# Optimization experiments

Hardware: AMD Instinct MI355X
Metric: run time of the kernel (lower is better)

## Reference

```python
import jax, jax.numpy as jnp
import numpy as np

WIDTH = 384
STEP_SIZE = 0.1  # hard-coded in EnergyBlock.__init__
EPS = 1e-5


def conv1d(x, w):
    # x: [B, Cin, L], w: [Cout, Cin, K], stride 1, SAME padding (padding=1 for k=3)
    return jax.lax.conv_general_dilated(
        x, w, window_strides=(1,), padding='SAME',
        dimension_numbers=('NCH', 'OIH', 'NCH'))


def layer_norm_cl(x):
    # torch layer_norm over shape[1:] == normalize jointly over (C, L) per batch elem,
    # no affine params, biased variance.
    mu = jnp.mean(x, axis=(1, 2), keepdims=True)
    var = jnp.mean(jnp.square(x - mu), axis=(1, 2), keepdims=True)
    return (x - mu) * jax.lax.rsqrt(var + EPS)


def energy_block(cat, op_w):
    # cat: [B, width+1, L] = concat(interim_thought, x)
    xl = layer_norm_cl(cat[:, :WIDTH])          # post-LN x (the grad variable)
    c = conv1d(cat, op_w)                        # operator(inputs): no path through xl
    # Ex = sum(c * xl) + sum(where(xl>=0, xl^2, 0))
    # dEx/dxl = c + 2*relu(xl)  (analytic; matches torch.autograd.grad)
    grads = c + 2.0 * jnp.maximum(xl, 0.0)
    return xl - STEP_SIZE * grads


def _init_conv(key, cout, cin, k=3):
    scale = (1.0 / (cin * k)) ** 0.5
    return jax.random.uniform(key, (cout, cin, k), jnp.float32, -scale, scale)


def setup_inputs() -> dict:
    key = jax.random.key(0)
    ks = jax.random.split(key, 6)
    B, L = 32, 512
    return {
        'x': jax.random.normal(ks[0], (B, 1, L), jnp.float32),
        'iters_to_do': 16,
        'proj_w': _init_conv(ks[1], WIDTH, 1),
        'op_w': _init_conv(ks[2], WIDTH, WIDTH + 1),
        'h1_w': _init_conv(ks[3], WIDTH, WIDTH),
        'h2_w': _init_conv(ks[4], WIDTH // 2, WIDTH),
        'h3_w': _init_conv(ks[5], 2, WIDTH // 2),
    }


def reference(x, iters_to_do, proj_w, op_w, h1_w, h2_w, h3_w):
    relu = jax.nn.relu
    interim = relu(conv1d(x, proj_w))  # initial_thought [B, width, L]

    def step(it, _):
        cat = jnp.concatenate([it, x], axis=1)       # recall=True
        new_it = energy_block(cat, op_w)
        out = conv1d(relu(conv1d(relu(conv1d(new_it, h1_w)), h2_w)), h3_w)  # [B,2,L]
        return new_it, out

    _, outs = jax.lax.scan(step, interim, None, length=iters_to_do)
    # eval mode: return all_outputs [B, iters, 2, L]
    return jnp.transpose(outs, (1, 0, 2, 3))
```

## Files before the change

### kernel.cpp

```cpp
#include <hip/hip_runtime.h>
#include <hip/hip_bf16.h>

#define BB 32
#define WW 384
#define LL 512
#define ITERS 16
#define NPB (WW * LL)
#define LROWS 514
#define RP (LROWS * 8)

typedef __attribute__((ext_vector_type(8))) short bf16x8;
typedef __attribute__((ext_vector_type(4))) float f32x4;

__device__ __forceinline__ float b2f(short s) {
    unsigned u = ((unsigned)(unsigned short)s) << 16;
    float f;
    __builtin_memcpy(&f, &u, 4);
    return f;
}
__device__ __forceinline__ short f2b(float v) {
    __hip_bfloat16 h = __float2bfloat16(v);
    return *(short*)&h;
}

__device__ __forceinline__ void gld16(const short* g, short* l) {
    __builtin_amdgcn_global_load_lds(
        (const __attribute__((address_space(1))) unsigned int*)g,
        (__attribute__((address_space(3))) unsigned int*)l, 16, 0, 0);
}

__global__ void wsplit_op(const float* __restrict__ w, short* __restrict__ wh) {
    int i = blockIdx.x * 256 + threadIdx.x;
    if (i >= 3 * 48 * 384 * 8) return;
    int e = i & 7, co = (i >> 3) % 384, oct = (i >> 3) / 384 % 48,
        tap = i / (8 * 384 * 48);
    int ci = oct * 8 + e;
    wh[i] = f2b(w[(co * 385 + ci) * 3 + tap]);
}

__global__ void wx_prep(const float* __restrict__ w, float* __restrict__ wx) {
    int i = blockIdx.x * 256 + threadIdx.x;
    if (i >= 3 * 384) return;
    int co = i % 384, tap = i / 384;
    wx[tap * 384 + co] = w[(co * 385 + 384) * 3 + tap];
}

__global__ void wsplit_h(const float* __restrict__ w, short* __restrict__ wh,
                         int COD, int CO_real) {
    int i = blockIdx.x * 256 + threadIdx.x;
    if (i >= 3 * 48 * COD * 8) return;
    int e = i & 7, co = (i >> 3) % COD, oct = (i >> 3) / COD % 48,
        tap = i / (8 * COD * 48);
    int ci = oct * 8 + e;
    float v = (co < CO_real) ? w[(co * 384 + ci) * 3 + tap] : 0.f;
    wh[i] = f2b(v);
}

__global__ void init_rows(short* itAh, short* itAl, short* itBh, short* itBl,
                          short* a1A, short* a1B, short* a2A, short* a2B) {
    int row = (blockIdx.x & 1) ? (LROWS - 1) : 0;
    int b = blockIdx.x >> 1;
    int tid = threadIdx.x;
    for (int i = tid; i < 48 * 8; i += 64) {
        size_t o = (size_t)b * 48 * RP + (size_t)(i >> 3) * RP + row * 8 + (i & 7);
        itAh[o] = 0; itAl[o] = 0; itBh[o] = 0; itBl[o] = 0;
        a1A[o] = 0; a1B[o] = 0;
    }
    for (int i = tid; i < 24 * 8; i += 64) {
        size_t o = (size_t)b * 24 * RP + (size_t)(i >> 3) * RP + row * 8 + (i & 7);
        a2A[o] = 0; a2B[o] = 0;
    }
}

__global__ void zero_part(float* part, int n) {
    int i = blockIdx.x * 256 + threadIdx.x;
    if (i < n) part[i] = 0.f;
}

__global__ __launch_bounds__(256) void proj_relu(const float* __restrict__ x,
                                                 const float* __restrict__ wp,
                                                 short* __restrict__ oh,
                                                 short* __restrict__ ol,
                                                 float* __restrict__ part) {
    int b = blockIdx.x >> 3, sl = blockIdx.x & 7;
    int tid = threadIdx.x;
    __shared__ float ws[WW * 3];
    __shared__ float xs[66];
    for (int i = tid; i < WW * 3; i += 256) ws[i] = wp[i];
    int l0 = sl * 64;
    for (int i = tid; i < 66; i += 256) {
        int l = l0 + i - 1;
        xs[i] = (l >= 0 && l < LL) ? x[b * LL + l] : 0.f;
    }
    __syncthreads();
    size_t sb = (size_t)b * 48 * RP;
    float s = 0.f, sq = 0.f;
    for (int idx = tid; idx < 64 * WW; idx += 256) {
        int lo = idx / WW, co = idx % WW;
        float v = fmaxf(ws[co * 3] * xs[lo] + ws[co * 3 + 1] * xs[lo + 1] +
                            ws[co * 3 + 2] * xs[lo + 2], 0.f);
        size_t o = sb + (size_t)(co >> 3) * RP + (l0 + lo + 1) * 8 + (co & 7);
        __hip_bfloat16 h = __float2bfloat16(v);
        oh[o] = *(short*)&h;
        ol[o] = f2b(v - __bfloat162float(h));
        s += v; sq += v * v;
    }
    #pragma unroll
    for (int off = 32; off > 0; off >>= 1) {
        s += __shfl_down(s, off);
        sq += __shfl_down(sq, off);
    }
    __shared__ float sr[8];
    int w = tid >> 6;
    if ((tid & 63) == 0) { sr[w] = s; sr[4 + w] = sq; }
    __syncthreads();
    if (tid == 0) {
        atomicAdd(&part[b * 2], sr[0] + sr[1] + sr[2] + sr[3]);
        atomicAdd(&part[b * 2 + 1], sr[4] + sr[5] + sr[6] + sr[7]);
    }
}


#define MMAC(A, B, MT, NT)                                                 \
    acc[MT][NT] = __builtin_amdgcn_mfma_f32_16x16x32_bf16(A, B,            \
                                                          acc[MT][NT], 0, 0, 0);

#define STAGE(KC, TB)                                                      \
    do {                                                                   \
        short* sb_ = smem + (TB) * (ASZ + BSZ);                            \
        _Pragma("unroll")                                                  \
        for (int r_ = 0; r_ < (ANS + 3) / 4; r_++) {                       \
            int s_ = r_ * 4 + wn;                                          \
            if (s_ < ANS) {                                                \
                int u0_ = s_ * 64;                                         \
                if (u0_ > AU - 64) u0_ = AU - 64;                          \
                int u_ = u0_ + lane;                                       \
                int oc_ = u_ / TLROWS;                                     \
                int rw_ = u_ - oc_ * TLROWS;                               \
                gld16(inh + ibase + (size_t)((KC) * 4 + oc_) * RP +        \
                          (size_t)(l0 + rw_) * 8,                          \
                      sb_ + u0_ * 8);                                      \
            }                                                              \
        }                                                                  \
        _Pragma("unroll")                                                  \
        for (int r_ = 0; r_ < BNS / 4; r_++) {                            \
            int u0_ = (r_ * 4 + wn) * 64;                                  \
            int t_ = u0_ / (4 * TCO);                                      \
            int rq_ = (u0_ / TCO) & 3;                                     \
            int co_ = (u0_ & (TCO - 1)) + lane;                            \
            gld16(wh + ((((size_t)t_ * CHUNKS + (KC)) * 4 + rq_) * COD +   \
                        co0 + co_) * 8,                                    \
                  sb_ + ASZ + u0_ * 8);                                    \
        }                                                                  \
    } while (0)

#define COMP_TAP(SB, T)                                                    \
    do {                                                                   \
        const short* As_ = (SB);                                           \
        const short* Bs_ = (SB) + ASZ;                                     \
        int ar_ = q * TLROWS + wl + lane15 + (T);                          \
        bf16x8 fa0 = *(const bf16x8*)(As_ + ar_ * 8);                      \
        bf16x8 fa1 = *(const bf16x8*)(As_ + (ar_ + 16) * 8);               \
        bf16x8 fa2 = *(const bf16x8*)(As_ + (ar_ + 32) * 8);               \
        bf16x8 fa3 = *(const bf16x8*)(As_ + (ar_ + 48) * 8);               \
        int br_ = ((T) * 4 + q) * TCO + wco + lane15;                      \
        bf16x8 fb0 = *(const bf16x8*)(Bs_ + br_ * 8);                      \
        bf16x8 fb1 = *(const bf16x8*)(Bs_ + (br_ + 16) * 8);               \
        bf16x8 fb2 = *(const bf16x8*)(Bs_ + (br_ + 32) * 8);               \
        bf16x8 fb3 = *(const bf16x8*)(Bs_ + (br_ + 48) * 8);               \
        MMAC(fa0, fb0, 0, 0) MMAC(fa0, fb1, 0, 1)                          \
        MMAC(fa0, fb2, 0, 2) MMAC(fa0, fb3, 0, 3)                          \
        MMAC(fa1, fb0, 1, 0) MMAC(fa1, fb1, 1, 1)                          \
        MMAC(fa1, fb2, 1, 2) MMAC(fa1, fb3, 1, 3)                          \
        MMAC(fa2, fb0, 2, 0) MMAC(fa2, fb1, 2, 1)                          \
        MMAC(fa2, fb2, 2, 2) MMAC(fa2, fb3, 2, 3)                          \
        MMAC(fa3, fb0, 3, 0) MMAC(fa3, fb1, 3, 1)                          \
        MMAC(fa3, fb2, 3, 2) MMAC(fa3, fb3, 3, 3)                          \
    } while (0)

template <int CHUNKS, int IOCT, int OOCT, int COD, int MODE, int LSPLIT>
__device__ __forceinline__ void conv_body(
    int bid, short* smem,
    const short* __restrict__ inh, const short* __restrict__ inl,
    const short* __restrict__ wh, const float* __restrict__ xf,
    const float* __restrict__ wx, const float* __restrict__ part_in,
    float* __restrict__ part_out, short* __restrict__ outh,
    short* __restrict__ outl) {
    constexpr int TLROWS = LSPLIT ? 258 : 130;
    constexpr int TCO = LSPLIT ? 64 : 128;
    constexpr int ASZ = 4 * TLROWS * 8;
    constexpr int BSZ = 12 * TCO * 8;
    constexpr int AU = 4 * TLROWS;
    constexpr int ANS = (AU + 63) / 64;
    constexpr int BNS = (12 * TCO) / 64;

    int tid = threadIdx.x;
    int lane = tid & 63;
    int wn = __builtin_amdgcn_readfirstlane(tid >> 6);
    int lane15 = lane & 15, q = lane >> 4;
    int b, l0, co0, wl, wco;
    if (LSPLIT) {
        int ct = bid >> 6, g = bid & 63;
        b = g >> 1; l0 = (g & 1) * 256; co0 = ct * 64;
        wl = wn * 64; wco = 0;
    } else {
        int ct = bid >> 7, g = bid & 127;
        b = g >> 2; l0 = (g & 3) * 128; co0 = ct * 128;
        wl = (wn >> 1) * 64; wco = (wn & 1) * 64;
    }
    const size_t ibase = (size_t)b * IOCT * RP;

    f32x4 acc[4][4];
    #pragma unroll
    for (int i = 0; i < 4; i++)
        #pragma unroll
        for (int j = 0; j < 4; j++) acc[i][j] = (f32x4){0.f, 0.f, 0.f, 0.f};

    STAGE(0, 0);
    __syncthreads();
    #pragma unroll 2
    for (int kc = 0; kc < CHUNKS; kc++) {
        int cur = kc & 1;
        if (kc + 1 < CHUNKS) STAGE(kc + 1, cur ^ 1);
        short* sb = smem + cur * (ASZ + BSZ);
        COMP_TAP(sb, 0);
        COMP_TAP(sb, 1);
        COMP_TAP(sb, 2);
        __syncthreads();
    }

    int l0w = l0 + wl, co0w = co0 + wco;
    const size_t obase = (size_t)b * OOCT * RP;
    if constexpr (MODE == 1) {
        float s_in = part_in[b * 2], sq_in = part_in[b * 2 + 1];
        float mu = s_in / (float)NPB;
        float var = sq_in / (float)NPB - mu * mu;
        float rs = rsqrtf(var + 1e-5f);
        const float* xb = xf + b * LL;
        float s = 0.f, sq = 0.f;
        #pragma unroll
        for (int nt = 0; nt < 4; nt++) {
            int n = co0w + nt * 16 + lane15;
            float w0 = wx[n], w1 = wx[384 + n], w2 = wx[768 + n];
            #pragma unroll
            for (int mt = 0; mt < 4; mt++)
                #pragma unroll
                for (int r = 0; r < 4; r++) {
                    int m = mt * 16 + q * 4 + r;
                    int l = l0w + m;
                    size_t idx = ibase + (size_t)(n >> 3) * RP +
                                 (l + 1) * 8 + (n & 7);
                    float xm1 = (l > 0) ? xb[l - 1] : 0.f;
                    float xp1 = (l < LL - 1) ? xb[l + 1] : 0.f;
                    float c = acc[mt][nt][r] + w0 * xm1 + w1 * xb[l] + w2 * xp1;
                    float itv = b2f(inh[idx]) + b2f(inl[idx]);
                    float xl = (itv - mu) * rs;
                    float nv = xl - 0.1f * c - 0.2f * fmaxf(xl, 0.f);
                    s += nv;
                    sq += nv * nv;
                    __hip_bfloat16 h = __float2bfloat16(nv);
                    outh[idx] = *(short*)&h;
                    outl[idx] = f2b(nv - __bfloat162float(h));
                }
        }
        #pragma unroll
        for (int off = 32; off > 0; off >>= 1) {
            s += __shfl_down(s, off);
            sq += __shfl_down(sq, off);
        }
        __shared__ float sr[8];
        if (lane == 0) { sr[wn] = s; sr[4 + wn] = sq; }
        __syncthreads();
        if (tid == 0) {
            atomicAdd(&part_out[b * 2], sr[0] + sr[1] + sr[2] + sr[3]);
            atomicAdd(&part_out[b * 2 + 1], sr[4] + sr[5] + sr[6] + sr[7]);
        }
    } else {
        #pragma unroll
        for (int mt = 0; mt < 4; mt++)
            #pragma unroll
            for (int nt = 0; nt < 4; nt++)
                #pragma unroll
                for (int r = 0; r < 4; r++) {
                    int m = mt * 16 + q * 4 + r;
                    int n = co0w + nt * 16 + lane15;
                    size_t idx = obase + (size_t)(n >> 3) * RP +
                                 (l0w + m + 1) * 8 + (n & 7);
                    outh[idx] = f2b(fmaxf(acc[mt][nt][r], 0.f));
                }
    }
}

__global__ __launch_bounds__(128) void h3k(const short* __restrict__ a2,
                                           const float* __restrict__ w3,
                                           float* __restrict__ out, int t) {
    __shared__ float ws3[2 * 192 * 3];
    int tid = threadIdx.x;
    for (int i = tid; i < 2 * 192 * 3; i += 128) ws3[i] = w3[i];
    __syncthreads();
    int b = blockIdx.x >> 3, sl = blockIdx.x & 7;
    int l = sl * 64 + (tid >> 1);
    int ch = tid & 1;
    const short* ab = a2 + (size_t)b * 24 * RP;
    const float* wc = ws3 + ch * 576;
    float a = 0.f;
    #pragma unroll 4
    for (int oct = 0; oct < 24; oct++) {
        const short* p = ab + (size_t)oct * RP + l * 8;
        bf16x8 v0 = *(const bf16x8*)p;
        bf16x8 v1 = *(const bf16x8*)(p + 8);
        bf16x8 v2 = *(const bf16x8*)(p + 16);
        #pragma unroll
        for (int j = 0; j < 8; j++) {
            const float* wp = wc + (oct * 8 + j) * 3;
            a += wp[0] * b2f(v0[j]) + wp[1] * b2f(v1[j]) + wp[2] * b2f(v2[j]);
        }
    }
    out[(((size_t)b * ITERS + t) * 2 + ch) * LL + l] = a;
}

__global__ __launch_bounds__(256, 2) void fusedF(
    const short* __restrict__ ch, const short* __restrict__ cl,
    short* __restrict__ nh, short* __restrict__ nl,
    const short* __restrict__ wOph, const short* __restrict__ wH1,
    const short* __restrict__ wH2, const float* __restrict__ xf,
    const float* __restrict__ wx, const float* __restrict__ part_in,
    float* __restrict__ part_out, short* __restrict__ a1w,
    const short* __restrict__ a1r, short* __restrict__ a2w,
    int opB, int h1B) {
    __shared__ __align__(16) short smem[2 * (4 * 130 * 8 + 12 * 128 * 8)];
    int bid = blockIdx.x;
    if (bid < opB) {
        conv_body<12, 48, 48, 384, 1, 0>(bid, smem, ch, cl, wOph, xf, wx,
                                         part_in, part_out, nh, nl);
    } else if (bid < opB + h1B) {
        conv_body<12, 48, 48, 384, 0, 0>(bid - opB, smem, ch, nullptr, wH1,
                                         nullptr, nullptr, nullptr, nullptr,
                                         a1w, nullptr);
    } else {
        conv_body<12, 48, 24, 192, 0, 1>(bid - opB - h1B, smem, a1r, nullptr,
                                         wH2, nullptr, nullptr, nullptr,
                                         nullptr, a2w, nullptr);
    }
}

extern "C" void kernel_launch(void* const* d_in, const int* in_sizes, int n_in,
                              void* d_out, int out_size, void* d_ws, size_t ws_size,
                              hipStream_t stream) {
    const float* x = (const float*)d_in[0];
    const float* proj_w = (const float*)d_in[2];
    const float* op_w = (const float*)d_in[3];
    const float* h1_w = (const float*)d_in[4];
    const float* h2_w = (const float*)d_in[5];
    const float* h3_w = (const float*)d_in[6];
    float* out = (float*)d_out;

    char* base = (char*)d_ws;
    size_t off = 0;
    auto alloc = [&](size_t bytes) {
        char* p = base + off;
        off += (bytes + 255) & ~(size_t)255;
        return p;
    };
    const size_t ITB = (size_t)BB * 48 * RP * 2;
    short* itAh = (short*)alloc(ITB);
    short* itAl = (short*)alloc(ITB);
    short* itBh = (short*)alloc(ITB);
    short* itBl = (short*)alloc(ITB);
    short* a1A = (short*)alloc((size_t)BB * 48 * RP * 2);
    short* a1B = (short*)alloc((size_t)BB * 48 * RP * 2);
    short* a2A = (short*)alloc((size_t)BB * 24 * RP * 2);
    short* a2B = (short*)alloc((size_t)BB * 24 * RP * 2);
    short* wOph = (short*)alloc((size_t)3 * 48 * 384 * 8 * 2);
    short* wH1 = (short*)alloc((size_t)3 * 48 * 384 * 8 * 2);
    short* wH2 = (short*)alloc((size_t)3 * 48 * 192 * 8 * 2);
    float* wx = (float*)alloc((size_t)3 * 384 * 4);
    float* part = (float*)alloc((size_t)(ITERS + 1) * 64 * 4);
    if (off > ws_size) return;

    wsplit_op<<<(3 * 48 * 384 * 8 + 255) / 256, 256, 0, stream>>>(op_w, wOph);
    wx_prep<<<5, 256, 0, stream>>>(op_w, wx);
    wsplit_h<<<(3 * 48 * 384 * 8 + 255) / 256, 256, 0, stream>>>(h1_w, wH1, 384, 384);
    wsplit_h<<<(3 * 48 * 192 * 8 + 255) / 256, 256, 0, stream>>>(h2_w, wH2, 192, 192);
    init_rows<<<BB * 2, 64, 0, stream>>>(itAh, itAl, itBh, itBl, a1A, a1B,
                                         a2A, a2B);
    zero_part<<<5, 256, 0, stream>>>(part, (ITERS + 1) * 64);
    proj_relu<<<BB * 8, 256, 0, stream>>>(x, proj_w, itAh, itAl, part);

    short* a1buf[2] = {a1A, a1B};
    short* a2buf[2] = {a2A, a2B};
    short *ch = itAh, *cl = itAl, *nh = itBh, *nl = itBl;
    for (int t = 0; t < ITERS + 2; t++) {
        int opB = (t < ITERS) ? 384 : 0;
        int h1B = (t >= 1 && t <= ITERS) ? 384 : 0;
        int h2B = (t >= 2 && t <= ITERS + 1) ? 192 : 0;
        int tp = (t < ITERS) ? t : 0;
        fusedF<<<opB + h1B + h2B, 256, 0, stream>>>(
            ch, cl, nh, nl, wOph, wH1, wH2, x, wx, part + tp * 64,
            part + (tp + 1) * 64, a1buf[(t - 1) & 1], a1buf[(t - 2) & 1],
            a2buf[(t - 2) & 1], opB, h1B);
        if (t >= 3)
            h3k<<<256, 128, 0, stream>>>(a2buf[(t - 3) & 1], h3_w, out, t - 3);
        if (t < ITERS) {
            short* th = ch; ch = nh; nh = th;
            short* tl = cl; cl = nl; nl = tl;
        }
    }
    h3k<<<256, 128, 0, stream>>>(a2buf[(ITERS - 1) & 1], h3_w, out, ITERS - 1);
}
```

Before: 1.095 ms.

## Load conv weight fragments directly from global memory instead of LDS staging

```diff
diff --git a/kernel.cpp b/kernel.cpp
--- a/kernel.cpp
+++ b/kernel.cpp
@@ -127,7 +127,7 @@
 
 #define STAGE(KC, TB)                                                      \
     do {                                                                   \
-        short* sb_ = smem + (TB) * (ASZ + BSZ);                            \
+        short* sb_ = smem + (TB) * ASZ;                                    \
         _Pragma("unroll")                                                  \
         for (int r_ = 0; r_ < (ANS + 3) / 4; r_++) {                       \
             int s_ = r_ * 4 + wn;                                          \
@@ -142,32 +142,22 @@
                       sb_ + u0_ * 8);                                      \
             }                                                              \
         }                                                                  \
-        _Pragma("unroll")                                                  \
-        for (int r_ = 0; r_ < BNS / 4; r_++) {                            \
-            int u0_ = (r_ * 4 + wn) * 64;                                  \
-            int t_ = u0_ / (4 * TCO);                                      \
-            int rq_ = (u0_ / TCO) & 3;                                     \
-            int co_ = (u0_ & (TCO - 1)) + lane;                            \
-            gld16(wh + ((((size_t)t_ * CHUNKS + (KC)) * 4 + rq_) * COD +   \
-                        co0 + co_) * 8,                                    \
-                  sb_ + ASZ + u0_ * 8);                                    \
-        }                                                                  \
     } while (0)
 
-#define COMP_TAP(SB, T)                                                    \
+#define COMP_TAP(SB, T, KC)                                                \
     do {                                                                   \
         const short* As_ = (SB);                                           \
-        const short* Bs_ = (SB) + ASZ;                                     \
         int ar_ = q * TLROWS + wl + lane15 + (T);                          \
         bf16x8 fa0 = *(const bf16x8*)(As_ + ar_ * 8);                      \
         bf16x8 fa1 = *(const bf16x8*)(As_ + (ar_ + 16) * 8);               \
         bf16x8 fa2 = *(const bf16x8*)(As_ + (ar_ + 32) * 8);               \
         bf16x8 fa3 = *(const bf16x8*)(As_ + (ar_ + 48) * 8);               \
-        int br_ = ((T) * 4 + q) * TCO + wco + lane15;                      \
-        bf16x8 fb0 = *(const bf16x8*)(Bs_ + br_ * 8);                      \
-        bf16x8 fb1 = *(const bf16x8*)(Bs_ + (br_ + 16) * 8);               \
-        bf16x8 fb2 = *(const bf16x8*)(Bs_ + (br_ + 32) * 8);               \
-        bf16x8 fb3 = *(const bf16x8*)(Bs_ + (br_ + 48) * 8);               \
+        const short* bp_ = wh + ((((size_t)(T) * CHUNKS + (KC)) * 4 + q) * \
+                                     COD + co0w + lane15) * 8;             \
+        bf16x8 fb0 = *(const bf16x8*)(bp_);                                \
+        bf16x8 fb1 = *(const bf16x8*)(bp_ + 16 * 8);                       \
+        bf16x8 fb2 = *(const bf16x8*)(bp_ + 32 * 8);                       \
+        bf16x8 fb3 = *(const bf16x8*)(bp_ + 48 * 8);                       \
         MMAC(fa0, fb0, 0, 0) MMAC(fa0, fb1, 0, 1)                          \
         MMAC(fa0, fb2, 0, 2) MMAC(fa0, fb3, 0, 3)                          \
         MMAC(fa1, fb0, 1, 0) MMAC(fa1, fb1, 1, 1)                          \
@@ -187,12 +177,9 @@
     float* __restrict__ part_out, short* __restrict__ outh,
     short* __restrict__ outl) {
     constexpr int TLROWS = LSPLIT ? 258 : 130;
-    constexpr int TCO = LSPLIT ? 64 : 128;
     constexpr int ASZ = 4 * TLROWS * 8;
-    constexpr int BSZ = 12 * TCO * 8;
     constexpr int AU = 4 * TLROWS;
     constexpr int ANS = (AU + 63) / 64;
-    constexpr int BNS = (12 * TCO) / 64;
 
     int tid = threadIdx.x;
     int lane = tid & 63;
@@ -208,6 +195,7 @@
         b = g >> 2; l0 = (g & 3) * 128; co0 = ct * 128;
         wl = (wn >> 1) * 64; wco = (wn & 1) * 64;
     }
+    const int co0w = co0 + wco;
     const size_t ibase = (size_t)b * IOCT * RP;
 
     f32x4 acc[4][4];
@@ -222,14 +210,14 @@
     for (int kc = 0; kc < CHUNKS; kc++) {
         int cur = kc & 1;
         if (kc + 1 < CHUNKS) STAGE(kc + 1, cur ^ 1);
-        short* sb = smem + cur * (ASZ + BSZ);
-        COMP_TAP(sb, 0);
-        COMP_TAP(sb, 1);
-        COMP_TAP(sb, 2);
+        short* sb = smem + cur * ASZ;
+        COMP_TAP(sb, 0, kc);
+        COMP_TAP(sb, 1, kc);
+        COMP_TAP(sb, 2, kc);
         __syncthreads();
     }
 
-    int l0w = l0 + wl, co0w = co0 + wco;
+    int l0w = l0 + wl;
     const size_t obase = (size_t)b * OOCT * RP;
     if constexpr (MODE == 1) {
         float s_in = part_in[b * 2], sq_in = part_in[b * 2 + 1];
@@ -319,7 +307,7 @@
     out[(((size_t)b * ITERS + t) * 2 + ch) * LL + l] = a;
 }
 
-__global__ __launch_bounds__(256, 2) void fusedF(
+__global__ __launch_bounds__(256, 3) void fusedF(
     const short* __restrict__ ch, const short* __restrict__ cl,
     short* __restrict__ nh, short* __restrict__ nl,
     const short* __restrict__ wOph, const short* __restrict__ wH1,
@@ -328,7 +316,7 @@
     float* __restrict__ part_out, short* __restrict__ a1w,
     const short* __restrict__ a1r, short* __restrict__ a2w,
     int opB, int h1B) {
-    __shared__ __align__(16) short smem[2 * (4 * 130 * 8 + 12 * 128 * 8)];
+    __shared__ __align__(16) short smem[2 * 4 * 258 * 8];
     int bid = blockIdx.x;
     if (bid < opB) {
         conv_body<12, 48, 48, 384, 1, 0>(bid, smem, ch, cl, wOph, xf, wx,
```

New measurement: 1.175 ms. 7.3% more time.
